# Performance work log

Measured on AMD Instinct MI355X. Metric: run time of the kernel, lower is better.

## Reference

```python
import jax, jax.numpy as jnp
import numpy as np

TRAN_DIM = 768
N_HEADS = 8
HEAD_DIM = 96
INNER = N_HEADS * HEAD_DIM  # 768


def setup_inputs() -> dict:
    key = jax.random.key(0)
    k1, k2, k3, k4, k5 = jax.random.split(key, 5)
    x = jax.random.normal(k1, (16, 1024, TRAN_DIM), dtype=jnp.float32)
    s_in = 1.0 / np.sqrt(TRAN_DIM)
    W_qkv = jax.random.uniform(k2, (TRAN_DIM, INNER * 3), jnp.float32, -s_in, s_in)
    b_qkv = jax.random.uniform(k3, (INNER * 3,), jnp.float32, -s_in, s_in)
    s_o = 1.0 / np.sqrt(INNER)
    W_out = jax.random.uniform(k4, (INNER, TRAN_DIM), jnp.float32, -s_o, s_o)
    b_out = jax.random.uniform(k5, (TRAN_DIM,), jnp.float32, -s_o, s_o)
    return {"x": x, "W_qkv": W_qkv, "b_qkv": b_qkv, "W_out": W_out, "b_out": b_out}


def reference(x, W_qkv, b_qkv, W_out, b_out):
    B, N, _ = x.shape
    qkv = x @ W_qkv + b_qkv  # [B, N, 3*INNER]
    q, k, v = jnp.split(qkv, 3, axis=-1)
    # [B, N, INNER] -> [B, H, N, D]
    def to_heads(t):
        return t.reshape(B, N, N_HEADS, HEAD_DIM).transpose(0, 2, 1, 3)
    q, k, v = to_heads(q), to_heads(k), to_heads(v)
    scale = HEAD_DIM ** (-0.5)
    dots = jnp.einsum('bhnd,bhmd->bhnm', q, k) * scale
    attn = jax.nn.softmax(dots, axis=-1)
    out = jnp.einsum('bhnm,bhmd->bhnd', attn, v)
    out = out.transpose(0, 2, 1, 3).reshape(B, N, INNER)
    return out @ W_out + b_out
```

## Files before the change

kernel.cpp:

```cpp
#include <hip/hip_runtime.h>
#include <hip/hip_bf16.h>


#define DEVINL __device__ __forceinline__

typedef __attribute__((ext_vector_type(8))) short s16x8;
typedef __attribute__((ext_vector_type(4))) short s16x4;
typedef __attribute__((ext_vector_type(4))) float f32x4;
typedef __attribute__((ext_vector_type(16))) float f32x16;

DEVINL short f2bf(float f) {
  union { float f; unsigned u; } c; c.f = f;
  unsigned r = c.u + 0x7FFFu + ((c.u >> 16) & 1u);
  return (short)(r >> 16);
}
DEVINL float asf(unsigned u) {
  union { unsigned u; float f; } c; c.u = u; return c.f;
}
DEVINL unsigned pack2(float a, float b) {
  union { float f; unsigned u; } ca, cb; ca.f = a; cb.f = b;
  return (ca.u >> 16) | (cb.u & 0xffff0000u);
}
DEVINL int swap23(int k) { return (k & ~12) | ((k & 4) << 1) | ((k & 8) >> 1); }

DEVINL void gload_lds16(const short* g, short* lds) {
  __builtin_amdgcn_global_load_lds((const __attribute__((address_space(1))) void*)g,
                                   (__attribute__((address_space(3))) void*)lds, 16, 0, 0);
}


__global__ void cvt_x_kernel(const float* __restrict__ in, short* __restrict__ out) {
  int i = blockIdx.x * 256 + threadIdx.x;
  float4 v = ((const float4*)in)[i];
  s16x4 o = { f2bf(v.x), f2bf(v.y), f2bf(v.z), f2bf(v.w) };
  *(s16x4*)(out + (size_t)i * 4) = o;
}

__global__ void tcvt_kernel(const float* __restrict__ in, short* __restrict__ out, int R, int C) {
  __shared__ float t[32][33];
  int tx = threadIdx.x & 31, ty = threadIdx.x >> 5;
  int r0 = blockIdx.y * 32, c0 = blockIdx.x * 32;
#pragma unroll
  for (int i = 0; i < 4; i++) {
    int r = ty + i * 8;
    t[r][tx] = in[(size_t)(r0 + r) * C + c0 + tx];
  }
  __syncthreads();
#pragma unroll
  for (int i = 0; i < 4; i++) {
    int r = ty + i * 8;
    out[(size_t)(c0 + r) * R + r0 + tx] = f2bf(t[tx][r]);
  }
}

__global__ void vtrans_kernel(const short* __restrict__ qkvb, short* __restrict__ out) {
  __shared__ short t[32][34];
  int tx = threadIdx.x & 31, ty = threadIdx.x >> 5;
  int d0 = blockIdx.x * 32, n0 = blockIdx.y * 32;
  int pair = blockIdx.z;
  int b = pair >> 3, h = pair & 7;
#pragma unroll
  for (int i = 0; i < 4; i++) {
    int r = ty + i * 8;
    t[r][tx] = qkvb[(size_t)(b * 1024 + n0 + r) * 2304 + 1536 + h * 96 + d0 + tx];
  }
  __syncthreads();
  size_t obase = (size_t)pair * 96 * 1024;
#pragma unroll
  for (int i = 0; i < 4; i++) {
    int r = ty + i * 8;
    out[obase + (size_t)(d0 + r) * 1024 + n0 + tx] = t[tx][r];
  }
}


template <int MODE>
__global__ __launch_bounds__(512, 2) void gemm256(const short* __restrict__ A, const short* __restrict__ Bt,
                                                  const float* __restrict__ bias, int K, int nTn,
                                                  short* __restrict__ qkvb, float* __restrict__ outf) {
  __shared__ short lds[65536];
  short* const ldsA = lds;
  short* const ldsB = lds + 32768;
  const int tid = threadIdx.x;
  const int l = tid & 63, w = tid >> 6;
  const int lo = l & 15, hi = l >> 4;
  const int wm = w >> 2, wn = w & 3;

  int cpx = gridDim.x >> 3;
  int bid = blockIdx.x;
  int swz = (bid & 7) * cpx + (bid >> 3);
  int tm = swz / nTn, tn = swz - tm * nTn;

  const int NKT = K >> 6;
  const int NIT = NKT >> 1;

  const int rS = tid >> 3;
  const int ko = (((tid & 7) ^ (rS & 7)) << 3);
  const short* aS = A + (size_t)(tm * 256 + rS) * K + ko;
  const short* bS = Bt + (size_t)(tn * 256 + ((rS >> 5) << 6) + (rS & 31)) * K + ko;
  const size_t step128 = (size_t)128 * K;

  f32x4 acc[8][4] = {};

#define STAGE_A(kt, q, buf) do {                                        \
    const short* s_ = aS + (size_t)(q) * 64 * K + (kt) * 64;            \
    short* d_ = ldsA + ((buf) * 2 + (q)) * 8192 + tid * 8;              \
    gload_lds16(s_, d_); gload_lds16(s_ + step128, d_ + 4096); } while (0)
#define STAGE_B(kt, q, buf) do {                                        \
    const short* s_ = bS + (size_t)(q) * 32 * K + (kt) * 64;            \
    short* d_ = ldsB + ((buf) * 2 + (q)) * 8192 + tid * 8;              \
    gload_lds16(s_, d_); gload_lds16(s_ + step128, d_ + 4096); } while (0)

#define DS_A(AF, bufc, qm) do {                                                   \
    const short* p_ = ldsA + ((bufc) * 2 + (qm)) * 8192 + (wm * 64 + lo) * 64;    \
    _Pragma("unroll") for (int mi = 0; mi < 4; mi++)                              \
      _Pragma("unroll") for (int kk = 0; kk < 2; kk++)                            \
        AF[mi][kk] = *(const s16x8*)(p_ + mi * 1024 + (((kk * 4 + hi) ^ (lo & 7)) << 3)); } while (0)
#define DS_B(BF, bufc, qn) do {                                                   \
    const short* p_ = ldsB + ((bufc) * 2 + (qn)) * 8192 + (wn * 32 + lo) * 64;    \
    _Pragma("unroll") for (int ni = 0; ni < 2; ni++)                              \
      _Pragma("unroll") for (int kk = 0; kk < 2; kk++)                            \
        BF[ni][kk] = *(const s16x8*)(p_ + ni * 1024 + (((kk * 4 + hi) ^ (lo & 7)) << 3)); } while (0)

#define BAR() do { __builtin_amdgcn_sched_barrier(0); __builtin_amdgcn_s_barrier(); \
                   __builtin_amdgcn_sched_barrier(0); } while (0)
#define MFMA16(qm, qn, AF, BF) do {                                               \
    __builtin_amdgcn_s_setprio(1);                                                \
    _Pragma("unroll") for (int kk = 0; kk < 2; kk++)                              \
      _Pragma("unroll") for (int mi = 0; mi < 4; mi++)                            \
        _Pragma("unroll") for (int ni = 0; ni < 2; ni++)                          \
          acc[(qm) * 4 + mi][(qn) * 2 + ni] = __builtin_amdgcn_mfma_f32_16x16x32_bf16( \
              AF[mi][kk], BF[ni][kk], acc[(qm) * 4 + mi][(qn) * 2 + ni], 0, 0, 0); \
    __builtin_amdgcn_s_setprio(0);                                                \
    __builtin_amdgcn_sched_barrier(0); } while (0)

  STAGE_A(0, 0, 0); STAGE_B(0, 0, 0);
  STAGE_A(0, 1, 0); STAGE_B(0, 1, 0);
  STAGE_A(1, 0, 1); STAGE_B(1, 0, 1);
  asm volatile("s_waitcnt vmcnt(4)" ::: "memory");
  __builtin_amdgcn_s_barrier();

  s16x8 af[4][2], bfa[2][2], bfb[2][2];
#pragma unroll 1
  for (int i = 0; i < NIT; i++) {
    int T = 2 * i;
    bool last = (i == NIT - 1);
    DS_A(af, 0, 0); DS_B(bfa, 0, 0);
    if (T + 1 < NKT) STAGE_A(T + 1, 1, 1);
    BAR(); MFMA16(0, 0, af, bfa); BAR();
    DS_B(bfb, 0, 1);
    if (T + 1 < NKT) STAGE_B(T + 1, 1, 1);
    BAR(); MFMA16(0, 1, af, bfb); BAR();
    DS_A(af, 0, 1);
    if (T + 2 < NKT) STAGE_A(T + 2, 0, 0);
    BAR(); MFMA16(1, 0, af, bfa); BAR();
    if (T + 2 < NKT) STAGE_B(T + 2, 0, 0);
    BAR(); MFMA16(1, 1, af, bfb);
    if (last) { asm volatile("s_waitcnt vmcnt(0)" ::: "memory"); }
    else      { asm volatile("s_waitcnt vmcnt(4)" ::: "memory"); }
    BAR();
    DS_A(af, 1, 0); DS_B(bfa, 1, 0);
    if (T + 2 < NKT) STAGE_A(T + 2, 1, 0);
    BAR(); MFMA16(0, 0, af, bfa); BAR();
    DS_B(bfb, 1, 1);
    if (T + 2 < NKT) STAGE_B(T + 2, 1, 0);
    BAR(); MFMA16(0, 1, af, bfb); BAR();
    DS_A(af, 1, 1);
    if (T + 3 < NKT) STAGE_A(T + 3, 0, 1);
    BAR(); MFMA16(1, 0, af, bfa); BAR();
    if (T + 3 < NKT) STAGE_B(T + 3, 0, 1);
    BAR(); MFMA16(1, 1, af, bfb);
    if (!last) { asm volatile("s_waitcnt vmcnt(4)" ::: "memory"); }
    BAR();
  }
#undef STAGE_A
#undef STAGE_B
#undef DS_A
#undef DS_B
#undef BAR
#undef MFMA16

  if (MODE == 0) {
    const float qscale = 0.14724444757204526f;
#pragma unroll
    for (int ni = 0; ni < 4; ni++) {
      int colr = wn * 64 + ni * 16 + lo;
      int coln = tn * 256 + colr;
      float bv = bias[coln];
      float scl = (coln < 768) ? qscale : 1.0f;
#pragma unroll
      for (int mi = 0; mi < 8; mi++)
#pragma unroll
        for (int j = 0; j < 4; j++) {
          int rowr = wm * 128 + mi * 16 + hi * 4 + j;
          lds[rowr * 256 + colr] = f2bf((acc[mi][ni][j] + bv) * scl);
        }
    }
    __syncthreads();
    short* dstb = qkvb + (size_t)(tm * 256) * 2304 + tn * 256;
#pragma unroll
    for (int k = 0; k < 16; k++) {
      int g = k * 512 + tid;
      int r = g >> 5, c = g & 31;
      *(s16x8*)(dstb + (size_t)r * 2304 + c * 8) = *(const s16x8*)(lds + r * 256 + c * 8);
    }
  } else {
#pragma unroll
    for (int ni = 0; ni < 4; ni++) {
      int coln = tn * 256 + wn * 64 + ni * 16 + lo;
      float bv = bias[coln];
#pragma unroll
      for (int mi = 0; mi < 8; mi++) {
#pragma unroll
        for (int j = 0; j < 4; j++) {
          int rowm = tm * 256 + wm * 128 + mi * 16 + hi * 4 + j;
          outf[(size_t)rowm * 768 + coln] = acc[mi][ni][j] + bv;
        }
      }
    }
  }
}


__global__ __launch_bounds__(256) void attn_kernel(const short* __restrict__ qkvb,
                                                   const short* __restrict__ vtb,
                                                   short* __restrict__ attn_out) {
  __shared__ short Ka[64 * 64];
  __shared__ short Kb[64 * 32];
  __shared__ short Vlds[96 * 64];
  int tid = threadIdx.x, lane = tid & 63, wid = tid >> 6;
  int q31 = lane & 31, hi2 = lane >> 5;
  int bid = blockIdx.x;
  int pair = bid & 127, qt = bid >> 7;
  int b = pair >> 3, h = pair & 7;
  const short* Vtp = vtb + (size_t)pair * 1024 * 96;
  int qrow0 = qt * 128 + wid * 32;

  s16x8 qf[6];
#pragma unroll
  for (int dc = 0; dc < 6; dc++)
    qf[dc] = *(const s16x8*)(qkvb + (size_t)(b * 1024 + qrow0 + q31) * 2304 +
                             h * 96 + dc * 16 + hi2 * 8);

  const short* sp[6];
  short* sdst[6];
  int sstep[6];
#pragma unroll
  for (int i = 0; i < 6; i++) {
    if (i < 3) {
      int c = i * 256 + tid;
      int krow = c / 12, kcc = c - krow * 12;
      int lam = swap23(krow);
      sdst[i] = (kcc < 8) ? Ka + lam * 64 + ((kcc ^ (lam & 7)) << 3)
                          : Kb + lam * 32 + (((kcc - 8) ^ (lam & 3)) << 3);
      sp[i] = qkvb + (size_t)(b * 1024 + krow) * 2304 + 768 + h * 96 + kcc * 8;
      sstep[i] = 64 * 2304;
    } else {
      int d = (i - 3) * 256 + tid;
      int vrow = d >> 3, vcc = d & 7;
      sdst[i] = Vlds + vrow * 64 + ((vcc ^ (vrow & 7)) << 3);
      sp[i] = Vtp + (size_t)vrow * 1024 + vcc * 8;
      sstep[i] = 64;
    }
  }

  f32x16 accO[3] = {};
  float lsum = 0.0f;

  s16x8 sreg[6];
#pragma unroll
  for (int i = 0; i < 6; i++) sreg[i] = *(const s16x8*)sp[i];

  for (int t = 0; t < 16; t++) {
    __syncthreads();
#pragma unroll
    for (int i = 0; i < 6; i++) *(s16x8*)sdst[i] = sreg[i];
    __syncthreads();

    int t2 = (t + 1) & 15;
#pragma unroll
    for (int i = 0; i < 6; i++)
      sreg[i] = *(const s16x8*)(sp[i] + (size_t)t2 * sstep[i]);

#pragma unroll
    for (int kb = 0; kb < 2; kb++) {
      f32x16 st = {};
#pragma unroll
      for (int dc = 0; dc < 6; dc++) {
        int c = dc * 2 + hi2;
        int lam = kb * 32 + q31;
        const short* kp = (c < 8) ? Ka + lam * 64 + ((c ^ (lam & 7)) << 3)
                                  : Kb + lam * 32 + (((c - 8) ^ (lam & 3)) << 3);
        s16x8 kf = *(const s16x8*)kp;
        st = __builtin_amdgcn_mfma_f32_32x32x16_bf16(kf, qf[dc], st, 0, 0, 0);
      }

      unsigned u[8];
#pragma unroll
      for (int i = 0; i < 8; i++) {
        float p0 = __builtin_amdgcn_exp2f(st[2 * i]);
        float p1 = __builtin_amdgcn_exp2f(st[2 * i + 1]);
        unsigned w = pack2(p0, p1);
        u[i] = w;
        lsum += asf(w << 16) + asf(w & 0xffff0000u);
      }

#pragma unroll
      for (int half = 0; half < 2; half++) {
        union { unsigned w[4]; s16x8 v; } pa;
#pragma unroll
        for (int wi = 0; wi < 4; wi++) pa.w[wi] = u[half * 4 + wi];
        int kc = kb * 2 + half;
#pragma unroll
        for (int db = 0; db < 3; db++) {
          int d = db * 32 + q31;
          s16x8 vf = *(const s16x8*)(Vlds + d * 64 + (((kc * 2 + hi2) ^ (d & 7)) << 3));
          accO[db] = __builtin_amdgcn_mfma_f32_32x32x16_bf16(pa.v, vf, accO[db], 0, 0, 0);
        }
      }
    }
  }

  float s = lsum + __shfl_xor(lsum, 32, 64);
  float rinv = 1.0f / s;
  float rr[16];
#pragma unroll
  for (int r = 0; r < 16; r++)
    rr[r] = __shfl(rinv, (r & 3) + 8 * (r >> 2) + 4 * hi2, 64);

#pragma unroll
  for (int db = 0; db < 3; db++)
#pragma unroll
    for (int r = 0; r < 16; r++) {
      int qrow = qrow0 + (r & 3) + 8 * (r >> 2) + 4 * hi2;
      int d = db * 32 + q31;
      attn_out[((size_t)b * 1024 + qrow) * 768 + h * 96 + d] = f2bf(accO[db][r] * rr[r]);
    }
}


extern "C" void kernel_launch(void* const* d_in, const int* in_sizes, int n_in,
                              void* d_out, int out_size, void* d_ws, size_t ws_size,
                              hipStream_t stream) {
  const float* x = (const float*)d_in[0];
  const float* Wqkv = (const float*)d_in[1];
  const float* bqkv = (const float*)d_in[2];
  const float* Wout = (const float*)d_in[3];
  const float* bout = (const float*)d_in[4];
  float* out = (float*)d_out;

  char* ws = (char*)d_ws;
  short* xb = (short*)ws;
  short* wqkvT = (short*)(ws + 25165824);
  short* woutT = (short*)(ws + 28704768);
  short* qkvb = (short*)(ws + 29884416);
  short* vtb = (short*)(ws + 105381888);

  cvt_x_kernel<<<12288, 256, 0, stream>>>(x, xb);
  tcvt_kernel<<<dim3(72, 24), 256, 0, stream>>>(Wqkv, wqkvT, 768, 2304);
  tcvt_kernel<<<dim3(24, 24), 256, 0, stream>>>(Wout, woutT, 768, 768);

  gemm256<0><<<576, 512, 0, stream>>>(xb, wqkvT, bqkv, 768, 9, qkvb, nullptr);
  vtrans_kernel<<<dim3(3, 32, 128), 256, 0, stream>>>(qkvb, vtb);
  attn_kernel<<<1024, 256, 0, stream>>>(qkvb, vtb, xb);
  gemm256<1><<<192, 512, 0, stream>>>(xb, woutT, bout, 768, 3, nullptr, out);
}
```

Measured before the change: 208.4 us.

## Replace 256x256 GEMM tile with 256x128 tile and simpler double-buffered K pipeline

Both projection GEMMs switch from a 256x256 output tile with a 64-wide K step and quadrant-staged pipeline to a 256x128 tile with a 32-wide K step and a simpler double-buffered loop. Per-block LDS is halved and launch bounds allow four blocks per CU. Grid sizes double, giving more blocks for the small output projection (192 to 384) and better CU fill. The cost is lower operand reuse per tile, more global loads of A, and a different LDS swizzle and sync pattern.

```diff
diff --git a/kernel.cpp b/kernel.cpp
--- a/kernel.cpp
+++ b/kernel.cpp
@@ -75,148 +75,138 @@
 
 
 template <int MODE>
-__global__ __launch_bounds__(512, 2) void gemm256(const short* __restrict__ A, const short* __restrict__ Bt,
-                                                  const float* __restrict__ bias, int K, int nTn,
-                                                  short* __restrict__ qkvb, float* __restrict__ outf) {
-  __shared__ short lds[65536];
+__global__ __launch_bounds__(512, 4) void gemm2(const short* __restrict__ A, const short* __restrict__ Bt,
+                                                const float* __restrict__ bias, int K, int nTn,
+                                                short* __restrict__ qkvb, float* __restrict__ outf) {
+  __shared__ short lds[32768];
   short* const ldsA = lds;
-  short* const ldsB = lds + 32768;
+  short* const ldsB = lds + 16384;
   const int tid = threadIdx.x;
   const int l = tid & 63, w = tid >> 6;
   const int lo = l & 15, hi = l >> 4;
-  const int wm = w >> 2, wn = w & 3;
+  const int wm = w >> 1, wn = w & 1;
 
   int cpx = gridDim.x >> 3;
   int bid = blockIdx.x;
   int swz = (bid & 7) * cpx + (bid >> 3);
   int tm = swz / nTn, tn = swz - tm * nTn;
 
-  const int NKT = K >> 6;
-  const int NIT = NKT >> 1;
-
-  const int rS = tid >> 3;
-  const int ko = (((tid & 7) ^ (rS & 7)) << 3);
-  const short* aS = A + (size_t)(tm * 256 + rS) * K + ko;
-  const short* bS = Bt + (size_t)(tn * 256 + ((rS >> 5) << 6) + (rS & 31)) * K + ko;
-  const size_t step128 = (size_t)128 * K;
-
-  f32x4 acc[8][4] = {};
-
-#define STAGE_A(kt, q, buf) do {                                        \
-    const short* s_ = aS + (size_t)(q) * 64 * K + (kt) * 64;            \
-    short* d_ = ldsA + ((buf) * 2 + (q)) * 8192 + tid * 8;              \
-    gload_lds16(s_, d_); gload_lds16(s_ + step128, d_ + 4096); } while (0)
-#define STAGE_B(kt, q, buf) do {                                        \
-    const short* s_ = bS + (size_t)(q) * 32 * K + (kt) * 64;            \
-    short* d_ = ldsB + ((buf) * 2 + (q)) * 8192 + tid * 8;              \
-    gload_lds16(s_, d_); gload_lds16(s_ + step128, d_ + 4096); } while (0)
-
-#define DS_A(AF, bufc, qm) do {                                                   \
-    const short* p_ = ldsA + ((bufc) * 2 + (qm)) * 8192 + (wm * 64 + lo) * 64;    \
-    _Pragma("unroll") for (int mi = 0; mi < 4; mi++)                              \
-      _Pragma("unroll") for (int kk = 0; kk < 2; kk++)                            \
-        AF[mi][kk] = *(const s16x8*)(p_ + mi * 1024 + (((kk * 4 + hi) ^ (lo & 7)) << 3)); } while (0)
-#define DS_B(BF, bufc, qn) do {                                                   \
-    const short* p_ = ldsB + ((bufc) * 2 + (qn)) * 8192 + (wn * 32 + lo) * 64;    \
-    _Pragma("unroll") for (int ni = 0; ni < 2; ni++)                              \
-      _Pragma("unroll") for (int kk = 0; kk < 2; kk++)                            \
-        BF[ni][kk] = *(const s16x8*)(p_ + ni * 1024 + (((kk * 4 + hi) ^ (lo & 7)) << 3)); } while (0)
-
-#define BAR() do { __builtin_amdgcn_sched_barrier(0); __builtin_amdgcn_s_barrier(); \
-                   __builtin_amdgcn_sched_barrier(0); } while (0)
-#define MFMA16(qm, qn, AF, BF) do {                                               \
-    __builtin_amdgcn_s_setprio(1);                                                \
-    _Pragma("unroll") for (int kk = 0; kk < 2; kk++)                              \
-      _Pragma("unroll") for (int mi = 0; mi < 4; mi++)                            \
-        _Pragma("unroll") for (int ni = 0; ni < 2; ni++)                          \
-          acc[(qm) * 4 + mi][(qn) * 2 + ni] = __builtin_amdgcn_mfma_f32_16x16x32_bf16( \
-              AF[mi][kk], BF[ni][kk], acc[(qm) * 4 + mi][(qn) * 2 + ni], 0, 0, 0); \
-    __builtin_amdgcn_s_setprio(0);                                                \
+  const int NKT = K >> 5;
+
+  const int Ls = tid >> 3, s7 = tid & 7;
+  const int pS = (s7 >> 2) & 1;
+  const int cS = (s7 & 3) ^ (Ls & 3);
+  const int rho = 2 * Ls + pS;
+  const int gA = ((rho >> 5) << 6) + (rho & 31);
+  const short* aS0 = A + (size_t)(tm * 256 + gA) * K + cS * 8;
+  const short* aS1 = aS0 + (size_t)32 * K;
+  const short* bS = Bt + (size_t)(tn * 128 + rho) * K + cS * 8;
+  short* const aD = ldsA + tid * 8;
+  short* const bD = ldsB + tid * 8;
+
+#define ST_A(j, q) gload_lds16(((q) ? aS1 : aS0) + (j) * 32, aD + (((j) & 1) * 2 + (q)) * 4096)
+#define ST_B(j)    gload_lds16(bS + (j) * 32, bD + ((j) & 1) * 4096)
+
+  const int LaBase = wm * 16 + (lo >> 1);
+  const int LbBase = wn * 32 + (lo >> 1);
+  const int pp = (lo & 1) << 2;
+
+  f32x4 acc[4][4] = {};
+
+#define RD_A(AF, buf, qm) do {                                                   \
+    const short* base_ = ldsA + ((buf) * 2 + (qm)) * 4096;                       \
+    _Pragma("unroll") for (int mi = 0; mi < 2; mi++) {                           \
+      int La_ = LaBase + mi * 8;                                                 \
+      AF[mi] = *(const s16x8*)(base_ + La_ * 64 + (((hi ^ (La_ & 3)) + pp) << 3)); } } while (0)
+#define RD_B(BF, buf) do {                                                       \
+    const short* base_ = ldsB + (buf) * 4096;                                    \
+    _Pragma("unroll") for (int b = 0; b < 4; b++) {                              \
+      int Lb_ = LbBase + b * 8;                                                  \
+      BF[b] = *(const s16x8*)(base_ + Lb_ * 64 + (((hi ^ (Lb_ & 3)) + pp) << 3)); } } while (0)
+
+#define MM8(a0, AF, BF) do {                                                     \
+    __builtin_amdgcn_s_setprio(1);                                               \
+    _Pragma("unroll") for (int mi = 0; mi < 2; mi++)                             \
+      _Pragma("unroll") for (int b = 0; b < 4; b++)                              \
+        acc[(a0) + mi][b] = __builtin_amdgcn_mfma_f32_16x16x32_bf16(             \
+            AF[mi], BF[b], acc[(a0) + mi][b], 0, 0, 0);                          \
+    __builtin_amdgcn_s_setprio(0);                                               \
     __builtin_amdgcn_sched_barrier(0); } while (0)
 
-  STAGE_A(0, 0, 0); STAGE_B(0, 0, 0);
-  STAGE_A(0, 1, 0); STAGE_B(0, 1, 0);
-  STAGE_A(1, 0, 1); STAGE_B(1, 0, 1);
-  asm volatile("s_waitcnt vmcnt(4)" ::: "memory");
+#define WAITV(n) asm volatile("s_waitcnt vmcnt(" #n ")" ::: "memory")
+#define BARR() do { __builtin_amdgcn_sched_barrier(0); __builtin_amdgcn_s_barrier(); \
+                    __builtin_amdgcn_sched_barrier(0); } while (0)
+
+  ST_A(0, 0); ST_A(0, 1); ST_B(0);
+  ST_A(1, 0); ST_B(1);
+  WAITV(2);
   __builtin_amdgcn_s_barrier();
 
-  s16x8 af[4][2], bfa[2][2], bfb[2][2];
+  s16x8 af[2], bf[4];
 #pragma unroll 1
-  for (int i = 0; i < NIT; i++) {
-    int T = 2 * i;
-    bool last = (i == NIT - 1);
-    DS_A(af, 0, 0); DS_B(bfa, 0, 0);
-    if (T + 1 < NKT) STAGE_A(T + 1, 1, 1);
-    BAR(); MFMA16(0, 0, af, bfa); BAR();
-    DS_B(bfb, 0, 1);
-    if (T + 1 < NKT) STAGE_B(T + 1, 1, 1);
-    BAR(); MFMA16(0, 1, af, bfb); BAR();
-    DS_A(af, 0, 1);
-    if (T + 2 < NKT) STAGE_A(T + 2, 0, 0);
-    BAR(); MFMA16(1, 0, af, bfa); BAR();
-    if (T + 2 < NKT) STAGE_B(T + 2, 0, 0);
-    BAR(); MFMA16(1, 1, af, bfb);
-    if (last) { asm volatile("s_waitcnt vmcnt(0)" ::: "memory"); }
-    else      { asm volatile("s_waitcnt vmcnt(4)" ::: "memory"); }
-    BAR();
-    DS_A(af, 1, 0); DS_B(bfa, 1, 0);
-    if (T + 2 < NKT) STAGE_A(T + 2, 1, 0);
-    BAR(); MFMA16(0, 0, af, bfa); BAR();
-    DS_B(bfb, 1, 1);
-    if (T + 2 < NKT) STAGE_B(T + 2, 1, 0);
-    BAR(); MFMA16(0, 1, af, bfb); BAR();
-    DS_A(af, 1, 1);
-    if (T + 3 < NKT) STAGE_A(T + 3, 0, 1);
-    BAR(); MFMA16(1, 0, af, bfa); BAR();
-    if (T + 3 < NKT) STAGE_B(T + 3, 0, 1);
-    BAR(); MFMA16(1, 1, af, bfb);
-    if (!last) { asm volatile("s_waitcnt vmcnt(4)" ::: "memory"); }
-    BAR();
-  }
-#undef STAGE_A
-#undef STAGE_B
-#undef DS_A
-#undef DS_B
-#undef BAR
-#undef MFMA16
+  for (int kt = 0; kt < NKT; kt++) {
+    int buf = kt & 1;
+    RD_A(af, buf, 0);
+    RD_B(bf, buf);
+    MM8(0, af, bf);
+    if (kt + 1 < NKT) ST_A(kt + 1, 1);
+    if (kt == NKT - 1) { WAITV(0); } else { WAITV(3); }
+    BARR();
+    RD_A(af, buf, 1);
+    MM8(2, af, bf);
+    if (kt + 2 < NKT) {
+      ST_A(kt + 2, 0); ST_B(kt + 2);
+      WAITV(3);
+    } else {
+      WAITV(0);
+    }
+    BARR();
+  }
+#undef ST_A
+#undef ST_B
+#undef RD_A
+#undef RD_B
+#undef MM8
+#undef WAITV
+#undef BARR
 
   if (MODE == 0) {
     const float qscale = 0.14724444757204526f;
-#pragma unroll
-    for (int ni = 0; ni < 4; ni++) {
-      int colr = wn * 64 + ni * 16 + lo;
-      int coln = tn * 256 + colr;
+    __syncthreads();
+#pragma unroll
+    for (int b = 0; b < 4; b++) {
+      int colr = wn * 64 + b * 16 + lo;
+      int coln = tn * 128 + colr;
       float bv = bias[coln];
       float scl = (coln < 768) ? qscale : 1.0f;
 #pragma unroll
-      for (int mi = 0; mi < 8; mi++)
+      for (int a = 0; a < 4; a++)
 #pragma unroll
         for (int j = 0; j < 4; j++) {
-          int rowr = wm * 128 + mi * 16 + hi * 4 + j;
-          lds[rowr * 256 + colr] = f2bf((acc[mi][ni][j] + bv) * scl);
+          int rowr = wm * 64 + a * 16 + hi * 4 + j;
+          lds[rowr * 128 + colr] = f2bf((acc[a][b][j] + bv) * scl);
         }
     }
     __syncthreads();
-    short* dstb = qkvb + (size_t)(tm * 256) * 2304 + tn * 256;
-#pragma unroll
-    for (int k = 0; k < 16; k++) {
+    short* dstb = qkvb + (size_t)(tm * 256) * 2304 + tn * 128;
+#pragma unroll
+    for (int k = 0; k < 8; k++) {
       int g = k * 512 + tid;
-      int r = g >> 5, c = g & 31;
-      *(s16x8*)(dstb + (size_t)r * 2304 + c * 8) = *(const s16x8*)(lds + r * 256 + c * 8);
+      int r = g >> 4, c = g & 15;
+      *(s16x8*)(dstb + (size_t)r * 2304 + c * 8) = *(const s16x8*)(lds + r * 128 + c * 8);
     }
   } else {
 #pragma unroll
-    for (int ni = 0; ni < 4; ni++) {
-      int coln = tn * 256 + wn * 64 + ni * 16 + lo;
+    for (int b = 0; b < 4; b++) {
+      int coln = tn * 128 + wn * 64 + b * 16 + lo;
       float bv = bias[coln];
 #pragma unroll
-      for (int mi = 0; mi < 8; mi++) {
+      for (int a = 0; a < 4; a++)
 #pragma unroll
         for (int j = 0; j < 4; j++) {
-          int rowm = tm * 256 + wm * 128 + mi * 16 + hi * 4 + j;
-          outf[(size_t)rowm * 768 + coln] = acc[mi][ni][j] + bv;
+          int rowm = tm * 256 + wm * 64 + a * 16 + hi * 4 + j;
+          outf[(size_t)rowm * 768 + coln] = acc[a][b][j] + bv;
         }
-      }
     }
   }
 }
@@ -360,8 +350,8 @@
   tcvt_kernel<<<dim3(72, 24), 256, 0, stream>>>(Wqkv, wqkvT, 768, 2304);
   tcvt_kernel<<<dim3(24, 24), 256, 0, stream>>>(Wout, woutT, 768, 768);
 
-  gemm256<0><<<576, 512, 0, stream>>>(xb, wqkvT, bqkv, 768, 9, qkvb, nullptr);
+  gemm2<0><<<1152, 512, 0, stream>>>(xb, wqkvT, bqkv, 768, 18, qkvb, nullptr);
   vtrans_kernel<<<dim3(3, 32, 128), 256, 0, stream>>>(qkvb, vtb);
   attn_kernel<<<1024, 256, 0, stream>>>(qkvb, vtb, xb);
-  gemm256<1><<<192, 512, 0, stream>>>(xb, woutT, bout, 768, 3, nullptr, out);
-}
+  gemm2<1><<<384, 512, 0, stream>>>(xb, woutT, bout, 768, 6, nullptr, out);
+}
```

Measured after the change: 198.4 us. 1.05x faster.
